# Optimization experiments

Hardware: AMD Instinct MI355X
Metric: run time of the kernel (lower is better)

The kernel has to match this reference:

```python
import jax, jax.numpy as jnp
import numpy as np

B = 128               # number of graphs in the batch
N_PER_GRAPH = 32768   # nodes per graph (equal-sized graphs -> static shapes)
N = B * N_PER_GRAPH
E = 4 * N
# PyG TopKPooling: k = ceil(ratio * nodes_in_graph)
K1, K2, K3 = 328, 33, 4  # ceil(0.01*32768), ceil(0.1*328), ceil(0.1*33)


def _topk_pool(x, w, k, num_graphs):
    """PyG TopKPooling (min_score=None, nonlinearity=tanh).
    score = tanh((x . w) / ||w||); keep top-k per graph; x_out = x[perm] * score[perm].
    Nodes are grouped contiguously per graph (sorted `batch`), equal graph sizes.
    """
    n = x.shape[0] // num_graphs
    s = jnp.tanh((x @ w) / jnp.linalg.norm(w))            # [N_cur]
    vals, idx = jax.lax.top_k(s.reshape(num_graphs, n), k)  # [B,k]
    xb = x.reshape(num_graphs, n, x.shape[-1])
    xs = jnp.take_along_axis(xb, idx[:, :, None], axis=1)   # gather kept nodes [B,k,F]
    return (xs * vals[:, :, None]).reshape(num_graphs * k, x.shape[-1])


def setup_inputs() -> dict:
    key = jax.random.key(0)
    ks = jax.random.split(key, 13)
    l1, l2, l3, l4 = 5, 64, 32, 8
    sc = 0.1
    return {
        "x": jax.random.normal(ks[0], (N, l1), jnp.float32),
        "edge_index": jax.random.randint(ks[1], (2, E), 0, N, jnp.int32),
        "batch": jnp.repeat(jnp.arange(B, dtype=jnp.int32), N_PER_GRAPH),
        "w1": jax.random.normal(ks[2], (l1,), jnp.float32) * sc,
        "W_ih": jax.random.normal(ks[3], (l2, l1), jnp.float32) * sc,
        "b_ih": jax.random.normal(ks[4], (l2,), jnp.float32) * sc,
        "b_hh": jax.random.normal(ks[5], (l2,), jnp.float32) * sc,
        "w2": jax.random.normal(ks[6], (l2,), jnp.float32) * sc,
        "W2": jax.random.normal(ks[7], (l3, l2), jnp.float32) * sc,
        "b2": jax.random.normal(ks[8], (l3,), jnp.float32) * sc,
        "w3": jax.random.normal(ks[9], (l3,), jnp.float32) * sc,
        "W3": jax.random.normal(ks[10], (l4, l3), jnp.float32) * sc,
        "b3": jax.random.normal(ks[11], (l4,), jnp.float32) * sc,
    }


def reference(x, edge_index, batch, w1, W_ih, b_ih, b_hh, w2, W2, b2, w3, W3, b3):
    # pool1 (ratio=0.01) -> RNNCell with h0=0: tanh(x W_ih^T + b_ih + b_hh)
    x = _topk_pool(x, w1, K1, B)
    x = jnp.tanh(x @ W_ih.T + b_ih + b_hh)
    # pool2 (ratio=0.1) -> relu(Linear)
    x = _topk_pool(x, w2, K2, B)
    x = jax.nn.relu(x @ W2.T + b2)
    # pool3 (ratio=0.1) -> Linear
    x = _topk_pool(x, w3, K3, B)
    return x @ W3.T + b3  # [B*K3, 8]
```

## Files before the change

kernel.cpp:

```cpp
#include <hip/hip_runtime.h>
#include <stdint.h>
#include <math.h>

constexpr int NPG = 32768;
constexpr int NGRAPH = 128;
constexpr int L1 = 5, L2 = 64, L3 = 32, L4 = 8;
constexpr int K1 = 328, K2 = 33, K3 = 4;
constexpr int SEGS = 16;
constexpr int CAP  = 64;

__device__ __forceinline__ uint32_t mono(float f) {
  uint32_t u = __float_as_uint(f);
  return (u & 0x80000000u) ? ~u : (u | 0x80000000u);
}
__device__ __forceinline__ float imono(uint32_t k) {
  uint32_t u = (k & 0x80000000u) ? (k ^ 0x80000000u) : ~k;
  return __uint_as_float(u);
}
__device__ __forceinline__ float fast_tanh(float x) {
  float e = __expf(2.0f * x);
  return 1.0f - 2.0f / (e + 1.0f);
}

__global__ __launch_bounds__(256) void score_kernel(
    const float* __restrict__ x, const float* __restrict__ w1,
    int* __restrict__ cnts, unsigned long long* __restrict__ cand) {
  __shared__ __align__(16) float sb[2048 * L1];
  __shared__ unsigned long long cb[CAP];
  __shared__ int s_n;
  __shared__ float s_tf;
  const int tid = threadIdx.x;
  const int g = blockIdx.x >> 4;
  const int bg = blockIdx.x & 15;
  if (tid == 0) {
    s_n = 0;
    float s = 0.f;
    for (int k = 0; k < L1; ++k) s += w1[k] * w1[k];
    s_tf = 2.2315f * sqrtf(s);
  }
  const float w10 = w1[0], w11 = w1[1], w12 = w1[2], w13 = w1[3], w14 = w1[4];
  const float4* src = (const float4*)(x + ((size_t)g * NPG + bg * 2048) * L1);
#pragma unroll
  for (int k = 0; k < 10; ++k)
    ((float4*)sb)[tid + 256 * k] = src[tid + 256 * k];
  __syncthreads();
  const float tf = s_tf;
#pragma unroll
  for (int p = 0; p < 4; ++p) {
    const int np = tid + 256 * p;
    const float* r = sb + np * 10;
    float d0 = r[0]*w10 + r[1]*w11 + r[2]*w12 + r[3]*w13 + r[4]*w14;
    float d1 = r[5]*w10 + r[6]*w11 + r[7]*w12 + r[8]*w13 + r[9]*w14;
    const int i0 = bg * 2048 + 2 * np;
    if (d0 >= tf) {
      int pos = atomicAdd(&s_n, 1);
      if (pos < CAP)
        cb[pos] = ((unsigned long long)mono(d0) << 16) | (unsigned)(65535 - i0);
    }
    if (d1 >= tf) {
      int pos = atomicAdd(&s_n, 1);
      if (pos < CAP)
        cb[pos] = ((unsigned long long)mono(d1) << 16) | (unsigned)(65535 - (i0 + 1));
    }
  }
  __syncthreads();
  const int n = s_n;
  if (tid == 0) cnts[g * SEGS + bg] = n;
  if (tid < CAP && tid < n)
    cand[((size_t)g * SEGS + bg) * CAP + tid] = cb[tid];
}

__global__ __launch_bounds__(1024, 1) void selmlp_kernel(
    const float* __restrict__ x, const int* __restrict__ cnts,
    const unsigned long long* __restrict__ cand,
    const float* __restrict__ w1, const float* __restrict__ W_ih,
    const float* __restrict__ b_ih, const float* __restrict__ b_hh,
    const float* __restrict__ w2, const float* __restrict__ W2,
    const float* __restrict__ b2, const float* __restrict__ w3,
    const float* __restrict__ W3, const float* __restrict__ b3,
    float* __restrict__ out) {
  __shared__ __align__(16) float hbuf[K1 * 65 + K2 * 68 + K2 * 33];
  __shared__ __align__(16) unsigned long long comp[1024];
  __shared__ __align__(16) unsigned long long sorted[512];
  __shared__ __align__(16) float fa[5672];
  __shared__ int soff[SEGS + 1];
  __shared__ int wred[16];
  __shared__ int s_fb, s_ctot, s_lo, s_hi, s_done, s_cnt;
  __shared__ uint32_t s_T;
  __shared__ float s_inv[3];

  float* xsel  = fa;
  float* sWihP = fa + 2624;
  float* sbih  = fa + 3136;
  float* sW2   = fa + 3200;
  float* sb2   = fa + 5280;
  float* sw2v  = fa + 5312;
  float* sw3v  = fa + 5376;
  float* sW3   = fa + 5408;
  float* sb3   = fa + 5664;

  const int tid = threadIdx.x;
  const int wid = tid >> 6;
  const int g = blockIdx.x;
  const float* xg = x + (size_t)g * NPG * L1;

  for (int i = tid; i < 512; i += 1024) {
    int o = i >> 3, k = i & 7;
    sWihP[i] = (k < L1) ? W_ih[o * L1 + k] : 0.f;
  }
  for (int i = tid; i < L2; i += 1024) { sbih[i] = b_ih[i] + b_hh[i]; sw2v[i] = w2[i]; }
  for (int i = tid; i < L3 * L2; i += 1024) sW2[(i >> 6) * 65 + (i & 63)] = W2[i];
  for (int i = tid; i < L3; i += 1024) { sb2[i] = b2[i]; sw3v[i] = w3[i]; }
  for (int i = tid; i < L4 * L3; i += 1024) sW3[i] = W3[i];
  for (int i = tid; i < L4; i += 1024) sb3[i] = b3[i];
  if (tid < 64) {
    float a = (tid < L1) ? w1[tid] : 0.f;
    float b = w2[tid];
    float c = (tid < L3) ? w3[tid] : 0.f;
    a *= a; b *= b; c *= c;
    for (int d = 1; d < 64; d <<= 1) {
      a += __shfl_xor(a, d); b += __shfl_xor(b, d); c += __shfl_xor(c, d);
    }
    if (tid == 0) {
      s_inv[0] = 1.f / sqrtf(a); s_inv[1] = 1.f / sqrtf(b); s_inv[2] = 1.f / sqrtf(c);
      s_cnt = 0; s_done = 0; s_lo = 0; s_hi = 0;
    }
  }
  if (tid < SEGS) soff[tid] = cnts[g * SEGS + tid];
  __syncthreads();
  if (tid == 0) {
    int off = 0, fb = 0;
    for (int s2 = 0; s2 < SEGS; ++s2) {
      int c = soff[s2];
      if (c > CAP) fb = 1;
      soff[s2] = off;
      off += c;
    }
    soff[SEGS] = off;
    if (off < K1 || off > 1024) fb = 1;
    s_fb = fb; s_ctot = off;
  }
  __syncthreads();

  if (!s_fb) {
    const int wl = tid & 63;
    if (wid < SEGS) {
      const int o = soff[wid], c = soff[wid + 1] - o;
      if (wl < c) comp[o + wl] = cand[((size_t)g * SEGS + wid) * CAP + wl];
    }
    const int ctot = s_ctot;
    const int nrk = (ctot + 7) & ~7;
    if (tid >= ctot && tid < nrk) comp[tid] = 0ULL;
    __syncthreads();
    if (tid < nrk) {
      unsigned long long c = comp[tid];
      int r = 0;
      for (int i = 0; i < nrk; i += 8) {
        ulonglong2 v0 = *(const ulonglong2*)&comp[i];
        ulonglong2 v1 = *(const ulonglong2*)&comp[i + 2];
        ulonglong2 v2 = *(const ulonglong2*)&comp[i + 4];
        ulonglong2 v3 = *(const ulonglong2*)&comp[i + 6];
        r += (v0.x > c) + (v0.y > c) + (v1.x > c) + (v1.y > c) +
             (v2.x > c) + (v2.y > c) + (v3.x > c) + (v3.y > c);
      }
      if (r < K1) sorted[r] = c;
    }
    __syncthreads();
  } else {
    const float w10 = w1[0], w11 = w1[1], w12 = w1[2], w13 = w1[3], w14 = w1[4];
    if (tid == 0) { s_lo = 0; s_hi = -1; s_done = 0; }
    __syncthreads();
    for (int it = 0; it < 36; ++it) {
      if (s_done) break;
      const uint32_t lo = (uint32_t)s_lo, hi = (uint32_t)s_hi;
      const uint32_t q = (uint32_t)(((unsigned long long)lo + (unsigned long long)hi) >> 1);
      int cc = 0;
      for (int m = 0; m < 32; ++m) {
        const int i = m * 1024 + tid;
        const float* r = xg + (size_t)i * L1;
        float dv = r[0]*w10 + r[1]*w11 + r[2]*w12 + r[3]*w13 + r[4]*w14;
        cc += (mono(dv) >= q);
      }
      for (int d = 1; d < 64; d <<= 1) cc += __shfl_xor(cc, d);
      if ((tid & 63) == 0) wred[wid] = cc;
      __syncthreads();
      if (tid == 0) {
        int tot = 0;
        for (int w = 0; w < 16; ++w) tot += wred[w];
        if (tot >= K1 && tot <= 1024) { s_T = q; s_done = 1; }
        else if ((uint32_t)s_hi - (uint32_t)s_lo <= 1u) { s_T = (uint32_t)s_lo; s_done = 1; }
        else if (tot > 1024) { s_lo = (int)q; }
        else                 { s_hi = (int)q; }
      }
      __syncthreads();
    }
    const uint32_t T = s_T;
    for (int m = 0; m < 32; ++m) {
      const int i = m * 1024 + tid;
      const float* r = xg + (size_t)i * L1;
      float dv = r[0]*w10 + r[1]*w11 + r[2]*w12 + r[3]*w13 + r[4]*w14;
      if (mono(dv) >= T) {
        int p = atomicAdd(&s_cnt, 1);
        if (p < 1024)
          comp[p] = ((unsigned long long)mono(dv) << 16) | (unsigned)(65535 - i);
      }
    }
    __syncthreads();
    int cnt = s_cnt; if (cnt > 1024) cnt = 1024;
    int nrk = (cnt + 7) & ~7; if (nrk < 8) nrk = 8;
    if (tid >= cnt && tid < nrk) comp[tid] = 0ULL;
    __syncthreads();
    if (tid < nrk) {
      unsigned long long c = comp[tid];
      int r = 0;
      for (int i = 0; i < nrk; i += 8) {
        ulonglong2 v0 = *(const ulonglong2*)&comp[i];
        ulonglong2 v1 = *(const ulonglong2*)&comp[i + 2];
        ulonglong2 v2 = *(const ulonglong2*)&comp[i + 4];
        ulonglong2 v3 = *(const ulonglong2*)&comp[i + 6];
        r += (v0.x > c) + (v0.y > c) + (v1.x > c) + (v1.y > c) +
             (v2.x > c) + (v2.y > c) + (v3.x > c) + (v3.y > c);
      }
      if (r < K1) sorted[r] = c;
    }
    __syncthreads();
  }

  const float inv1 = s_inv[0], inv2 = s_inv[1], inv3 = s_inv[2];

  for (int p = tid; p < K1 * 8; p += 1024) {
    int j = p >> 3, k = p & 7;
    unsigned long long c = sorted[j];
    int idx = 65535 - (int)(c & 0xFFFFu);
    float sc = fast_tanh(imono((uint32_t)(c >> 16)) * inv1);
    xsel[p] = (k < L1) ? xg[(size_t)idx * L1 + k] * sc : 0.f;
  }
  __syncthreads();
  {
    const int o = tid & 63;
    float wreg[8];
#pragma unroll
    for (int k = 0; k < 8; ++k) wreg[k] = sWihP[o * 8 + k];
    const float bias = sbih[o];
    for (int p = tid; p < K1 * L2; p += 1024) {
      int row = p >> 6;
      float4 xa = *(const float4*)&xsel[row * 8];
      float4 xb = *(const float4*)&xsel[row * 8 + 4];
      float acc = bias;
      acc += xa.x * wreg[0]; acc += xa.y * wreg[1]; acc += xa.z * wreg[2];
      acc += xa.w * wreg[3]; acc += xb.x * wreg[4]; acc += xb.y * wreg[5];
      acc += xb.z * wreg[6]; acc += xb.w * wreg[7];
      hbuf[row * 65 + o] = fast_tanh(acc);
    }
  }
  __syncthreads();

  for (int j = tid; j < 384; j += 1024) {
    unsigned long long c = 0ULL;
    if (j < K1) {
      const float* hr = hbuf + j * 65;
      float acc = 0.f;
      for (int k = 0; k < L2; ++k) acc += hr[k] * sw2v[k];
      c = ((unsigned long long)mono(acc) << 16) | (unsigned)(65535 - j);
    }
    comp[j] = c;
  }
  __syncthreads();
  if (tid < 384) {
    unsigned long long c = comp[tid];
    int r = 0;
    for (int i = 0; i < 384; i += 8) {
      ulonglong2 v0 = *(const ulonglong2*)&comp[i];
      ulonglong2 v1 = *(const ulonglong2*)&comp[i + 2];
      ulonglong2 v2 = *(const ulonglong2*)&comp[i + 4];
      ulonglong2 v3 = *(const ulonglong2*)&comp[i + 6];
      r += (v0.x > c) + (v0.y > c) + (v1.x > c) + (v1.y > c) +
           (v2.x > c) + (v2.y > c) + (v3.x > c) + (v3.y > c);
    }
    sorted[r] = c;
  }
  __syncthreads();

  float* x2f = hbuf + K1 * 65;
  for (int p = tid; p < K2 * L2; p += 1024) {
    int j = p >> 6, k = p & 63;
    unsigned long long c = sorted[j];
    int row = 65535 - (int)(c & 0xFFFFu);
    float sc = fast_tanh(imono((uint32_t)(c >> 16)) * inv2);
    x2f[j * 68 + k] = hbuf[row * 65 + k] * sc;
  }
  __syncthreads();

  float* yf = x2f + K2 * 68;
  for (int p = tid; p < K2 * L3; p += 1024) {
    int j = p >> 5, o = p & 31;
    const float4* xr4 = (const float4*)(x2f + j * 68);
    const float* wr = sW2 + o * 65;
    float acc = sb2[o];
#pragma unroll
    for (int m = 0; m < 16; ++m) {
      float4 v = xr4[m];
      acc += v.x * wr[4 * m];     acc += v.y * wr[4 * m + 1];
      acc += v.z * wr[4 * m + 2]; acc += v.w * wr[4 * m + 3];
    }
    yf[j * 33 + o] = fmaxf(acc, 0.f);
  }
  __syncthreads();

  for (int j = tid; j < 64; j += 1024) {
    unsigned long long c = 0ULL;
    if (j < K2) {
      const float* yr = yf + j * 33;
      float acc = 0.f;
      for (int k = 0; k < L3; ++k) acc += yr[k] * sw3v[k];
      c = ((unsigned long long)mono(acc) << 16) | (unsigned)(65535 - j);
    }
    comp[j] = c;
  }
  __syncthreads();
  if (tid < 64) {
    unsigned long long c = comp[tid];
    int r = 0;
    for (int i = 0; i < 64; i += 8) {
      ulonglong2 v0 = *(const ulonglong2*)&comp[i];
      ulonglong2 v1 = *(const ulonglong2*)&comp[i + 2];
      ulonglong2 v2 = *(const ulonglong2*)&comp[i + 4];
      ulonglong2 v3 = *(const ulonglong2*)&comp[i + 6];
      r += (v0.x > c) + (v0.y > c) + (v1.x > c) + (v1.y > c) +
           (v2.x > c) + (v2.y > c) + (v3.x > c) + (v3.y > c);
    }
    sorted[r] = c;
  }
  __syncthreads();

  for (int p = tid; p < K3 * L4; p += 1024) {
    int t = p >> 3, o = p & 7;
    unsigned long long c = sorted[t];
    int row = 65535 - (int)(c & 0xFFFFu);
    float sc = fast_tanh(imono((uint32_t)(c >> 16)) * inv3);
    const float* yr = yf + row * 33;
    const float* wr = sW3 + o * L3;
    float acc = sb3[o];
    for (int k = 0; k < L3; ++k) acc += yr[k] * sc * wr[k];
    out[((size_t)g * K3 + t) * L4 + o] = acc;
  }
}

extern "C" void kernel_launch(void* const* d_in, const int* in_sizes, int n_in,
                              void* d_out, int out_size, void* d_ws, size_t ws_size,
                              hipStream_t stream) {
  const float* x    = (const float*)d_in[0];
  const float* w1   = (const float*)d_in[3];
  const float* W_ih = (const float*)d_in[4];
  const float* b_ih = (const float*)d_in[5];
  const float* b_hh = (const float*)d_in[6];
  const float* w2   = (const float*)d_in[7];
  const float* W2   = (const float*)d_in[8];
  const float* b2   = (const float*)d_in[9];
  const float* w3   = (const float*)d_in[10];
  const float* W3   = (const float*)d_in[11];
  const float* b3   = (const float*)d_in[12];
  float* out = (float*)d_out;

  int* cnts = (int*)d_ws;
  unsigned long long* cand =
      (unsigned long long*)((char*)d_ws + 8192);

  score_kernel<<<dim3(NGRAPH * SEGS), dim3(256), 0, stream>>>(x, w1, cnts, cand);
  selmlp_kernel<<<dim3(NGRAPH), dim3(1024), 0, stream>>>(
      x, cnts, cand, w1, W_ih, b_ih, b_hh, w2, W2, b2, w3, W3, b3, out);
}
```

Measured before the change: 45.26 us.

## Fuse score and select/MLP stages into one cooperative kernel with grid sync

Replaces the two-kernel pipeline with one cooperative launch of 256 blocks of 1024 threads. Each pair of blocks scores half a graph, then a grid-wide sync hands off to one block per graph for selection and the MLP stages. The goal is to remove the second launch and the gap between kernels. The cost is fewer, larger blocks streaming x through LDS staging, plus a grid barrier, and it falls back to the old path if the cooperative launch fails.

After: 171.4 us. 3.79x slower.

```diff
diff --git a/kernel.cpp b/kernel.cpp
--- a/kernel.cpp
+++ b/kernel.cpp
@@ -1,13 +1,15 @@
 #include <hip/hip_runtime.h>
+#include <hip/hip_cooperative_groups.h>
 #include <stdint.h>
 #include <math.h>
+
+namespace cg = cooperative_groups;
 
 constexpr int NPG = 32768;
 constexpr int NGRAPH = 128;
 constexpr int L1 = 5, L2 = 64, L3 = 32, L4 = 8;
 constexpr int K1 = 328, K2 = 33, K3 = 4;
-constexpr int SEGS = 16;
-constexpr int CAP  = 64;
+constexpr int HCAP = 512;
 
 __device__ __forceinline__ uint32_t mono(float f) {
   uint32_t u = __float_as_uint(f);
@@ -21,6 +23,311 @@
   float e = __expf(2.0f * x);
   return 1.0f - 2.0f / (e + 1.0f);
 }
+
+__global__ __launch_bounds__(1024, 1) void fused_coop(
+    const float* __restrict__ x,
+    const float* __restrict__ w1, const float* __restrict__ W_ih,
+    const float* __restrict__ b_ih, const float* __restrict__ b_hh,
+    const float* __restrict__ w2, const float* __restrict__ W2,
+    const float* __restrict__ b2, const float* __restrict__ w3,
+    const float* __restrict__ W3, const float* __restrict__ b3,
+    int* __restrict__ cnts, unsigned long long* __restrict__ cand,
+    float* __restrict__ out) {
+  __shared__ __align__(16) float arena[33400];
+  __shared__ int wred[16];
+  __shared__ int s_n, s_fb, s_ctot, s_lo, s_hi, s_done, s_cnt, s_c0;
+  __shared__ uint32_t s_T;
+  __shared__ float s_inv[3], s_tf;
+
+  float* hbuf = arena;
+  unsigned long long* comp = (unsigned long long*)(arena + 24656);
+  unsigned long long* sorted = (unsigned long long*)(arena + 26704);
+  float* fa = arena + 27728;
+  float* xsel  = fa;
+  float* sWihP = fa + 2624;
+  float* sbih  = fa + 3136;
+  float* sW2   = fa + 3200;
+  float* sb2   = fa + 5280;
+  float* sw2v  = fa + 5312;
+  float* sw3v  = fa + 5376;
+  float* sW3   = fa + 5408;
+  float* sb3   = fa + 5664;
+
+  const int tid = threadIdx.x;
+  const int bid = blockIdx.x;
+  const int g1 = bid >> 1, half = bid & 1;
+
+  for (int i = tid; i < 512; i += 1024) {
+    int o = i >> 3, k = i & 7;
+    sWihP[i] = (k < L1) ? W_ih[o * L1 + k] : 0.f;
+  }
+  for (int i = tid; i < L2; i += 1024) { sbih[i] = b_ih[i] + b_hh[i]; sw2v[i] = w2[i]; }
+  for (int i = tid; i < L3 * L2; i += 1024) sW2[(i >> 6) * 65 + (i & 63)] = W2[i];
+  for (int i = tid; i < L3; i += 1024) { sb2[i] = b2[i]; sw3v[i] = w3[i]; }
+  for (int i = tid; i < L4 * L3; i += 1024) sW3[i] = W3[i];
+  for (int i = tid; i < L4; i += 1024) sb3[i] = b3[i];
+  if (tid < 64) {
+    float a = (tid < L1) ? w1[tid] : 0.f;
+    float b = w2[tid];
+    float c = (tid < L3) ? w3[tid] : 0.f;
+    a *= a; b *= b; c *= c;
+    for (int d = 1; d < 64; d <<= 1) {
+      a += __shfl_xor(a, d); b += __shfl_xor(b, d); c += __shfl_xor(c, d);
+    }
+    if (tid == 0) {
+      float nw1 = sqrtf(a);
+      s_tf = 2.2315f * nw1;
+      s_inv[0] = 1.f / nw1; s_inv[1] = 1.f / sqrtf(b); s_inv[2] = 1.f / sqrtf(c);
+      s_n = 0; s_cnt = 0; s_done = 0;
+    }
+  }
+  const float w10 = w1[0], w11 = w1[1], w12 = w1[2], w13 = w1[3], w14 = w1[4];
+
+  {
+    float* stage = arena;
+    unsigned long long* cb = (unsigned long long*)(arena + 20480);
+    const float4* src = (const float4*)(x + ((size_t)g1 * NPG + half * 16384) * L1);
+    __syncthreads();
+    const float tf = s_tf;
+    for (int c = 0; c < 4; ++c) {
+#pragma unroll
+      for (int q = 0; q < 5; ++q)
+        ((float4*)stage)[tid + 1024 * q] = src[c * 5120 + tid + 1024 * q];
+      __syncthreads();
+      const float* r = stage + tid * 20;
+      const int i0 = half * 16384 + c * 4096 + tid * 4;
+#pragma unroll
+      for (int n = 0; n < 4; ++n) {
+        float d = r[n*5]*w10 + r[n*5+1]*w11 + r[n*5+2]*w12 + r[n*5+3]*w13 + r[n*5+4]*w14;
+        if (d >= tf) {
+          int pos = atomicAdd(&s_n, 1);
+          if (pos < HCAP)
+            cb[pos] = ((unsigned long long)mono(d) << 16) | (unsigned)(65535 - (i0 + n));
+        }
+      }
+      __syncthreads();
+    }
+    const int n = s_n;
+    if (tid == 0) cnts[bid] = n;
+    if (tid < HCAP && tid < n) cand[(size_t)bid * HCAP + tid] = cb[tid];
+  }
+  __threadfence();
+  cg::this_grid().sync();
+  if (bid >= NGRAPH) return;
+
+  const int g = bid;
+  const float* xg = x + (size_t)g * NPG * L1;
+  __threadfence();
+  if (tid == 0) {
+    int c0 = cnts[2 * g], c1 = cnts[2 * g + 1];
+    int fb = (c0 > HCAP || c1 > HCAP) ? 1 : 0;
+    int tot = c0 + c1;
+    if (tot < K1 || tot > 1024) fb = 1;
+    s_fb = fb; s_ctot = tot; s_c0 = c0;
+    s_lo = 0; s_hi = -1; s_done = 0; s_cnt = 0;
+  }
+  __syncthreads();
+
+  if (!s_fb) {
+    const int ctot = s_ctot, c0 = s_c0;
+    if (tid < c0)            comp[tid] = cand[(size_t)(2 * g) * HCAP + tid];
+    else if (tid < ctot)     comp[tid] = cand[(size_t)(2 * g + 1) * HCAP + (tid - c0)];
+    const int nrk = (ctot + 7) & ~7;
+    if (tid >= ctot && tid < nrk) comp[tid] = 0ULL;
+    __syncthreads();
+    if (tid < nrk) {
+      unsigned long long c = comp[tid];
+      int r = 0;
+      for (int i = 0; i < nrk; i += 8) {
+        ulonglong2 v0 = *(const ulonglong2*)&comp[i];
+        ulonglong2 v1 = *(const ulonglong2*)&comp[i + 2];
+        ulonglong2 v2 = *(const ulonglong2*)&comp[i + 4];
+        ulonglong2 v3 = *(const ulonglong2*)&comp[i + 6];
+        r += (v0.x > c) + (v0.y > c) + (v1.x > c) + (v1.y > c) +
+             (v2.x > c) + (v2.y > c) + (v3.x > c) + (v3.y > c);
+      }
+      if (r < K1) sorted[r] = c;
+    }
+    __syncthreads();
+  } else {
+    for (int it = 0; it < 36; ++it) {
+      if (s_done) break;
+      const uint32_t lo = (uint32_t)s_lo, hi = (uint32_t)s_hi;
+      const uint32_t q = (uint32_t)(((unsigned long long)lo + (unsigned long long)hi) >> 1);
+      int cc = 0;
+      for (int m = 0; m < 32; ++m) {
+        const int i = m * 1024 + tid;
+        const float* r = xg + (size_t)i * L1;
+        float dv = r[0]*w10 + r[1]*w11 + r[2]*w12 + r[3]*w13 + r[4]*w14;
+        cc += (mono(dv) >= q);
+      }
+      for (int d = 1; d < 64; d <<= 1) cc += __shfl_xor(cc, d);
+      if ((tid & 63) == 0) wred[tid >> 6] = cc;
+      __syncthreads();
+      if (tid == 0) {
+        int tot = 0;
+        for (int w = 0; w < 16; ++w) tot += wred[w];
+        if (tot >= K1 && tot <= 1024) { s_T = q; s_done = 1; }
+        else if ((uint32_t)s_hi - (uint32_t)s_lo <= 1u) { s_T = (uint32_t)s_lo; s_done = 1; }
+        else if (tot > 1024) { s_lo = (int)q; }
+        else                 { s_hi = (int)q; }
+      }
+      __syncthreads();
+    }
+    const uint32_t T = s_T;
+    for (int m = 0; m < 32; ++m) {
+      const int i = m * 1024 + tid;
+      const float* r = xg + (size_t)i * L1;
+      float dv = r[0]*w10 + r[1]*w11 + r[2]*w12 + r[3]*w13 + r[4]*w14;
+      if (mono(dv) >= T) {
+        int p = atomicAdd(&s_cnt, 1);
+        if (p < 1024)
+          comp[p] = ((unsigned long long)mono(dv) << 16) | (unsigned)(65535 - i);
+      }
+    }
+    __syncthreads();
+    int cnt = s_cnt; if (cnt > 1024) cnt = 1024;
+    int nrk = (cnt + 7) & ~7; if (nrk < 8) nrk = 8;
+    if (tid >= cnt && tid < nrk) comp[tid] = 0ULL;
+    __syncthreads();
+    if (tid < nrk) {
+      unsigned long long c = comp[tid];
+      int r = 0;
+      for (int i = 0; i < nrk; i += 8) {
+        ulonglong2 v0 = *(const ulonglong2*)&comp[i];
+        ulonglong2 v1 = *(const ulonglong2*)&comp[i + 2];
+        ulonglong2 v2 = *(const ulonglong2*)&comp[i + 4];
+        ulonglong2 v3 = *(const ulonglong2*)&comp[i + 6];
+        r += (v0.x > c) + (v0.y > c) + (v1.x > c) + (v1.y > c) +
+             (v2.x > c) + (v2.y > c) + (v3.x > c) + (v3.y > c);
+      }
+      if (r < K1) sorted[r] = c;
+    }
+    __syncthreads();
+  }
+
+  const float inv1 = s_inv[0], inv2 = s_inv[1], inv3 = s_inv[2];
+
+  for (int p = tid; p < K1 * 8; p += 1024) {
+    int j = p >> 3, k = p & 7;
+    unsigned long long c = sorted[j];
+    int idx = 65535 - (int)(c & 0xFFFFu);
+    float sc = fast_tanh(imono((uint32_t)(c >> 16)) * inv1);
+    xsel[p] = (k < L1) ? xg[(size_t)idx * L1 + k] * sc : 0.f;
+  }
+  __syncthreads();
+  {
+    const int o = tid & 63;
+    float wreg[8];
+#pragma unroll
+    for (int k = 0; k < 8; ++k) wreg[k] = sWihP[o * 8 + k];
+    const float bias = sbih[o];
+    for (int p = tid; p < K1 * L2; p += 1024) {
+      int row = p >> 6;
+      float4 xa = *(const float4*)&xsel[row * 8];
+      float4 xb = *(const float4*)&xsel[row * 8 + 4];
+      float acc = bias;
+      acc += xa.x * wreg[0]; acc += xa.y * wreg[1]; acc += xa.z * wreg[2];
+      acc += xa.w * wreg[3]; acc += xb.x * wreg[4]; acc += xb.y * wreg[5];
+      acc += xb.z * wreg[6]; acc += xb.w * wreg[7];
+      hbuf[row * 65 + o] = fast_tanh(acc);
+    }
+  }
+  __syncthreads();
+
+  for (int j = tid; j < 384; j += 1024) {
+    unsigned long long c = 0ULL;
+    if (j < K1) {
+      const float* hr = hbuf + j * 65;
+      float acc = 0.f;
+      for (int k = 0; k < L2; ++k) acc += hr[k] * sw2v[k];
+      c = ((unsigned long long)mono(acc) << 16) | (unsigned)(65535 - j);
+    }
+    comp[j] = c;
+  }
+  __syncthreads();
+  if (tid < 384) {
+    unsigned long long c = comp[tid];
+    int r = 0;
+    for (int i = 0; i < 384; i += 8) {
+      ulonglong2 v0 = *(const ulonglong2*)&comp[i];
+      ulonglong2 v1 = *(const ulonglong2*)&comp[i + 2];
+      ulonglong2 v2 = *(const ulonglong2*)&comp[i + 4];
+      ulonglong2 v3 = *(const ulonglong2*)&comp[i + 6];
+      r += (v0.x > c) + (v0.y > c) + (v1.x > c) + (v1.y > c) +
+           (v2.x > c) + (v2.y > c) + (v3.x > c) + (v3.y > c);
+    }
+    sorted[r] = c;
+  }
+  __syncthreads();
+
+  float* x2f = hbuf + K1 * 65;
+  for (int p = tid; p < K2 * L2; p += 1024) {
+    int j = p >> 6, k = p & 63;
+    unsigned long long c = sorted[j];
+    int row = 65535 - (int)(c & 0xFFFFu);
+    float sc = fast_tanh(imono((uint32_t)(c >> 16)) * inv2);
+    x2f[j * 68 + k] = hbuf[row * 65 + k] * sc;
+  }
+  __syncthreads();
+
+  float* yf = x2f + K2 * 68;
+  for (int p = tid; p < K2 * L3; p += 1024) {
+    int j = p >> 5, o = p & 31;
+    const float4* xr4 = (const float4*)(x2f + j * 68);
+    const float* wr = sW2 + o * 65;
+    float acc = sb2[o];
+#pragma unroll
+    for (int m = 0; m < 16; ++m) {
+      float4 v = xr4[m];
+      acc += v.x * wr[4 * m];     acc += v.y * wr[4 * m + 1];
+      acc += v.z * wr[4 * m + 2]; acc += v.w * wr[4 * m + 3];
+    }
+    yf[j * 33 + o] = fmaxf(acc, 0.f);
+  }
+  __syncthreads();
+
+  for (int j = tid; j < 64; j += 1024) {
+    unsigned long long c = 0ULL;
+    if (j < K2) {
+      const float* yr = yf + j * 33;
+      float acc = 0.f;
+      for (int k = 0; k < L3; ++k) acc += yr[k] * sw3v[k];
+      c = ((unsigned long long)mono(acc) << 16) | (unsigned)(65535 - j);
+    }
+    comp[j] = c;
+  }
+  __syncthreads();
+  if (tid < 64) {
+    unsigned long long c = comp[tid];
+    int r = 0;
+    for (int i = 0; i < 64; i += 8) {
+      ulonglong2 v0 = *(const ulonglong2*)&comp[i];
+      ulonglong2 v1 = *(const ulonglong2*)&comp[i + 2];
+      ulonglong2 v2 = *(const ulonglong2*)&comp[i + 4];
+      ulonglong2 v3 = *(const ulonglong2*)&comp[i + 6];
+      r += (v0.x > c) + (v0.y > c) + (v1.x > c) + (v1.y > c) +
+           (v2.x > c) + (v2.y > c) + (v3.x > c) + (v3.y > c);
+    }
+    sorted[r] = c;
+  }
+  __syncthreads();
+
+  for (int p = tid; p < K3 * L4; p += 1024) {
+    int t = p >> 3, o = p & 7;
+    unsigned long long c = sorted[t];
+    int row = 65535 - (int)(c & 0xFFFFu);
+    float sc = fast_tanh(imono((uint32_t)(c >> 16)) * inv3);
+    const float* yr = yf + row * 33;
+    const float* wr = sW3 + o * L3;
+    float acc = sb3[o];
+    for (int k = 0; k < L3; ++k) acc += yr[k] * sc * wr[k];
+    out[((size_t)g * K3 + t) * L4 + o] = acc;
+  }
+}
+
+constexpr int SEGS = 16;
+constexpr int CAP  = 64;
 
 __global__ __launch_bounds__(256) void score_kernel(
     const float* __restrict__ x, const float* __restrict__ w1,
@@ -366,7 +673,15 @@
   unsigned long long* cand =
       (unsigned long long*)((char*)d_ws + 8192);
 
-  score_kernel<<<dim3(NGRAPH * SEGS), dim3(256), 0, stream>>>(x, w1, cnts, cand);
-  selmlp_kernel<<<dim3(NGRAPH), dim3(1024), 0, stream>>>(
-      x, cnts, cand, w1, W_ih, b_ih, b_hh, w2, W2, b2, w3, W3, b3, out);
+  void* args[] = { (void*)&x, (void*)&w1, (void*)&W_ih, (void*)&b_ih,
+                   (void*)&b_hh, (void*)&w2, (void*)&W2, (void*)&b2,
+                   (void*)&w3, (void*)&W3, (void*)&b3,
+                   (void*)&cnts, (void*)&cand, (void*)&out };
+  hipError_t err = hipLaunchCooperativeKernel(
+      (const void*)fused_coop, dim3(2 * NGRAPH), dim3(1024), args, 0, stream);
+  if (err != hipSuccess) {
+    score_kernel<<<dim3(NGRAPH * SEGS), dim3(256), 0, stream>>>(x, w1, cnts, cand);
+    selmlp_kernel<<<dim3(NGRAPH), dim3(1024), 0, stream>>>(
+        x, cnts, cand, w1, W_ih, b_ih, b_hh, w2, W2, b2, w3, W3, b3, out);
+  }
 }
```

## Compute RNN hidden states and pool2 scores for candidates in score kernel

Applied to the files above, without the earlier changes.

The score kernel now evaluates the RNNCell (tanh of W_ih·x plus bias) and the pool2 score for every top-k candidate it finds, spread across all 2048 blocks. It writes the hidden states and scores to a workspace slot per candidate. The per-graph selection kernel then runs pool2 directly on those precomputed scores and gathers only the 33 kept hidden rows, skipping its serial xsel/hidden-layer phases. The cost is extra global traffic: writing hidden vectors for all candidates, not just the 328 kept ones. The path also depends on the workspace being large enough, and falls back to the old path otherwise.

New measurement: 49.99 us. 1.1x slower.

```diff
diff --git a/kernel.cpp b/kernel.cpp
--- a/kernel.cpp
+++ b/kernel.cpp
@@ -8,6 +8,7 @@
 constexpr int K1 = 328, K2 = 33, K3 = 4;
 constexpr int SEGS = 16;
 constexpr int CAP  = 64;
+constexpr int SLOTS = SEGS * CAP;
 
 __device__ __forceinline__ uint32_t mono(float f) {
   uint32_t u = __float_as_uint(f);
@@ -24,11 +25,18 @@
 
 __global__ __launch_bounds__(256) void score_kernel(
     const float* __restrict__ x, const float* __restrict__ w1,
-    int* __restrict__ cnts, unsigned long long* __restrict__ cand) {
+    const float* __restrict__ W_ih, const float* __restrict__ b_ih,
+    const float* __restrict__ b_hh, const float* __restrict__ w2,
+    int* __restrict__ cnts, unsigned long long* __restrict__ cand,
+    float* __restrict__ s2g, float* __restrict__ hG, int hasH) {
   __shared__ __align__(16) float sb[2048 * L1];
   __shared__ unsigned long long cb[CAP];
+  __shared__ float xs[CAP * L1];
+  __shared__ float sWih[L2 * L1];
+  __shared__ float sbih[L2];
+  __shared__ float sw2[L2];
   __shared__ int s_n;
-  __shared__ float s_tf;
+  __shared__ float s_tf, s_inv1;
   const int tid = threadIdx.x;
   const int g = blockIdx.x >> 4;
   const int bg = blockIdx.x & 15;
@@ -36,8 +44,12 @@
     s_n = 0;
     float s = 0.f;
     for (int k = 0; k < L1; ++k) s += w1[k] * w1[k];
-    s_tf = 2.2315f * sqrtf(s);
-  }
+    float nw = sqrtf(s);
+    s_tf = 2.2315f * nw;
+    s_inv1 = 1.f / nw;
+  }
+  for (int i = tid; i < L2 * L1; i += 256) sWih[i] = W_ih[i];
+  for (int i = tid; i < L2; i += 256) { sbih[i] = b_ih[i] + b_hh[i]; sw2[i] = w2[i]; }
   const float w10 = w1[0], w11 = w1[1], w12 = w1[2], w13 = w1[3], w14 = w1[4];
   const float4* src = (const float4*)(x + ((size_t)g * NPG + bg * 2048) * L1);
 #pragma unroll
@@ -65,14 +77,40 @@
   }
   __syncthreads();
   const int n = s_n;
+  const int nn = n < CAP ? n : CAP;
   if (tid == 0) cnts[g * SEGS + bg] = n;
   if (tid < CAP && tid < n)
     cand[((size_t)g * SEGS + bg) * CAP + tid] = cb[tid];
+  if (!hasH) return;
+  for (int p = tid; p < nn * L1; p += 256) {
+    int ci = p / L1, k = p - ci * L1;
+    unsigned long long c = cb[ci];
+    int i = 65535 - (int)(c & 0xFFFFu);
+    int local = i - bg * 2048;
+    float sc = fast_tanh(imono((uint32_t)(c >> 16)) * s_inv1);
+    xs[p] = sb[local * L1 + k] * sc;
+  }
+  __syncthreads();
+  for (int p = tid; p < nn * 64; p += 256) {
+    int ci = p >> 6, o = p & 63;
+    const float* xr = xs + ci * L1;
+    const float* wr = sWih + o * L1;
+    float acc = sbih[o];
+#pragma unroll
+    for (int k = 0; k < L1; ++k) acc += xr[k] * wr[k];
+    float h = fast_tanh(acc);
+    const int slot = bg * CAP + ci;
+    hG[((size_t)g * SLOTS + slot) * 64 + o] = h;
+    float term = h * sw2[o];
+    for (int d = 1; d < 64; d <<= 1) term += __shfl_xor(term, d);
+    if (o == 0) s2g[(size_t)g * SLOTS + slot] = term;
+  }
 }
 
 __global__ __launch_bounds__(1024, 1) void selmlp_kernel(
     const float* __restrict__ x, const int* __restrict__ cnts,
     const unsigned long long* __restrict__ cand,
+    const float* __restrict__ s2g, const float* __restrict__ hG, int hasH,
     const float* __restrict__ w1, const float* __restrict__ W_ih,
     const float* __restrict__ b_ih, const float* __restrict__ b_hh,
     const float* __restrict__ w2, const float* __restrict__ W2,
@@ -83,6 +121,8 @@
   __shared__ __align__(16) unsigned long long comp[1024];
   __shared__ __align__(16) unsigned long long sorted[512];
   __shared__ __align__(16) float fa[5672];
+  __shared__ int slotarr[1024];
+  __shared__ int slotof[512];
   __shared__ int soff[SEGS + 1];
   __shared__ int wred[16];
   __shared__ int s_fb, s_ctot, s_lo, s_hi, s_done, s_cnt;
@@ -129,7 +169,7 @@
   if (tid < SEGS) soff[tid] = cnts[g * SEGS + tid];
   __syncthreads();
   if (tid == 0) {
-    int off = 0, fb = 0;
+    int off = 0, fb = hasH ? 0 : 1;
     for (int s2 = 0; s2 < SEGS; ++s2) {
       int c = soff[s2];
       if (c > CAP) fb = 1;
@@ -142,11 +182,18 @@
   }
   __syncthreads();
 
+  const float inv1 = s_inv[0], inv2 = s_inv[1], inv3 = s_inv[2];
+  float* x2f = hbuf + K1 * 65;
+  float* yf  = x2f + K2 * 68;
+
   if (!s_fb) {
     const int wl = tid & 63;
     if (wid < SEGS) {
       const int o = soff[wid], c = soff[wid + 1] - o;
-      if (wl < c) comp[o + wl] = cand[((size_t)g * SEGS + wid) * CAP + wl];
+      if (wl < c) {
+        comp[o + wl] = cand[((size_t)g * SEGS + wid) * CAP + wl];
+        slotarr[o + wl] = wid * CAP + wl;
+      }
     }
     const int ctot = s_ctot;
     const int nrk = (ctot + 7) & ~7;
@@ -163,7 +210,38 @@
         r += (v0.x > c) + (v0.y > c) + (v1.x > c) + (v1.y > c) +
              (v2.x > c) + (v2.y > c) + (v3.x > c) + (v3.y > c);
       }
-      if (r < K1) sorted[r] = c;
+      if (r < K1) slotof[r] = slotarr[tid];
+    }
+    __syncthreads();
+    for (int j = tid; j < 384; j += 1024) {
+      unsigned long long c = 0ULL;
+      if (j < K1) {
+        float s2 = s2g[(size_t)g * SLOTS + slotof[j]];
+        c = ((unsigned long long)mono(s2) << 16) | (unsigned)(65535 - j);
+      }
+      comp[j] = c;
+    }
+    __syncthreads();
+    if (tid < 384) {
+      unsigned long long c = comp[tid];
+      int r = 0;
+      for (int i = 0; i < 384; i += 8) {
+        ulonglong2 v0 = *(const ulonglong2*)&comp[i];
+        ulonglong2 v1 = *(const ulonglong2*)&comp[i + 2];
+        ulonglong2 v2 = *(const ulonglong2*)&comp[i + 4];
+        ulonglong2 v3 = *(const ulonglong2*)&comp[i + 6];
+        r += (v0.x > c) + (v0.y > c) + (v1.x > c) + (v1.y > c) +
+             (v2.x > c) + (v2.y > c) + (v3.x > c) + (v3.y > c);
+      }
+      sorted[r] = c;
+    }
+    __syncthreads();
+    for (int p = tid; p < K2 * L2; p += 1024) {
+      int j = p >> 6, k = p & 63;
+      unsigned long long c = sorted[j];
+      int row = 65535 - (int)(c & 0xFFFFu);
+      float sc = fast_tanh(imono((uint32_t)(c >> 16)) * inv2);
+      x2f[j * 68 + k] = hG[((size_t)g * SLOTS + slotof[row]) * 64 + k] * sc;
     }
     __syncthreads();
   } else {
@@ -224,74 +302,67 @@
       if (r < K1) sorted[r] = c;
     }
     __syncthreads();
-  }
-
-  const float inv1 = s_inv[0], inv2 = s_inv[1], inv3 = s_inv[2];
-
-  for (int p = tid; p < K1 * 8; p += 1024) {
-    int j = p >> 3, k = p & 7;
-    unsigned long long c = sorted[j];
-    int idx = 65535 - (int)(c & 0xFFFFu);
-    float sc = fast_tanh(imono((uint32_t)(c >> 16)) * inv1);
-    xsel[p] = (k < L1) ? xg[(size_t)idx * L1 + k] * sc : 0.f;
-  }
-  __syncthreads();
-  {
-    const int o = tid & 63;
-    float wreg[8];
+    for (int p = tid; p < K1 * 8; p += 1024) {
+      int j = p >> 3, k = p & 7;
+      unsigned long long c = sorted[j];
+      int idx = 65535 - (int)(c & 0xFFFFu);
+      float sc = fast_tanh(imono((uint32_t)(c >> 16)) * inv1);
+      xsel[p] = (k < L1) ? xg[(size_t)idx * L1 + k] * sc : 0.f;
+    }
+    __syncthreads();
+    {
+      const int o = tid & 63;
+      float wreg[8];
 #pragma unroll
-    for (int k = 0; k < 8; ++k) wreg[k] = sWihP[o * 8 + k];
-    const float bias = sbih[o];
-    for (int p = tid; p < K1 * L2; p += 1024) {
-      int row = p >> 6;
-      float4 xa = *(const float4*)&xsel[row * 8];
-      float4 xb = *(const float4*)&xsel[row * 8 + 4];
-      float acc = bias;
-      acc += xa.x * wreg[0]; acc += xa.y * wreg[1]; acc += xa.z * wreg[2];
-      acc += xa.w * wreg[3]; acc += xb.x * wreg[4]; acc += xb.y * wreg[5];
-      acc += xb.z * wreg[6]; acc += xb.w * wreg[7];
-      hbuf[row * 65 + o] = fast_tanh(acc);
-    }
-  }
-  __syncthreads();
-
-  for (int j = tid; j < 384; j += 1024) {
-    unsigned long long c = 0ULL;
-    if (j < K1) {
-      const float* hr = hbuf + j * 65;
-      float acc = 0.f;
-      for (int k = 0; k < L2; ++k) acc += hr[k] * sw2v[k];
-      c = ((unsigned long long)mono(acc) << 16) | (unsigned)(65535 - j);
-    }
-    comp[j] = c;
-  }
-  __syncthreads();
-  if (tid < 384) {
-    unsigned long long c = comp[tid];
-    int r = 0;
-    for (int i = 0; i < 384; i += 8) {
-      ulonglong2 v0 = *(const ulonglong2*)&comp[i];
-      ulonglong2 v1 = *(const ulonglong2*)&comp[i + 2];
-      ulonglong2 v2 = *(const ulonglong2*)&comp[i + 4];
-      ulonglong2 v3 = *(const ulonglong2*)&comp[i + 6];
-      r += (v0.x > c) + (v0.y > c) + (v1.x > c) + (v1.y > c) +
-           (v2.x > c) + (v2.y > c) + (v3.x > c) + (v3.y > c);
-    }
-    sorted[r] = c;
-  }
-  __syncthreads();
-
-  float* x2f = hbuf + K1 * 65;
-  for (int p = tid; p < K2 * L2; p += 1024) {
-    int j = p >> 6, k = p & 63;
-    unsigned long long c = sorted[j];
-    int row = 65535 - (int)(c & 0xFFFFu);
-    float sc = fast_tanh(imono((uint32_t)(c >> 16)) * inv2);
-    x2f[j * 68 + k] = hbuf[row * 65 + k] * sc;
-  }
-  __syncthreads();
-
-  float* yf = x2f + K2 * 68;
+      for (int k = 0; k < 8; ++k) wreg[k] = sWihP[o * 8 + k];
+      const float bias = sbih[o];
+      for (int p = tid; p < K1 * L2; p += 1024) {
+        int row = p >> 6;
+        float4 xa = *(const float4*)&xsel[row * 8];
+        float4 xb = *(const float4*)&xsel[row * 8 + 4];
+        float acc = bias;
+        acc += xa.x * wreg[0]; acc += xa.y * wreg[1]; acc += xa.z * wreg[2];
+        acc += xa.w * wreg[3]; acc += xb.x * wreg[4]; acc += xb.y * wreg[5];
+        acc += xb.z * wreg[6]; acc += xb.w * wreg[7];
+        hbuf[row * 65 + o] = fast_tanh(acc);
+      }
+    }
+    __syncthreads();
+    for (int j = tid; j < 384; j += 1024) {
+      unsigned long long c = 0ULL;
+      if (j < K1) {
+        const float* hr = hbuf + j * 65;
+        float acc = 0.f;
+        for (int k = 0; k < L2; ++k) acc += hr[k] * sw2v[k];
+        c = ((unsigned long long)mono(acc) << 16) | (unsigned)(65535 - j);
+      }
+      comp[j] = c;
+    }
+    __syncthreads();
+    if (tid < 384) {
+      unsigned long long c = comp[tid];
+      int r = 0;
+      for (int i = 0; i < 384; i += 8) {
+        ulonglong2 v0 = *(const ulonglong2*)&comp[i];
+        ulonglong2 v1 = *(const ulonglong2*)&comp[i + 2];
+        ulonglong2 v2 = *(const ulonglong2*)&comp[i + 4];
+        ulonglong2 v3 = *(const ulonglong2*)&comp[i + 6];
+        r += (v0.x > c) + (v0.y > c) + (v1.x > c) + (v1.y > c) +
+             (v2.x > c) + (v2.y > c) + (v3.x > c) + (v3.y > c);
+      }
+      sorted[r] = c;
+    }
+    __syncthreads();
+    for (int p = tid; p < K2 * L2; p += 1024) {
+      int j = p >> 6, k = p & 63;
+      unsigned long long c = sorted[j];
+      int row = 65535 - (int)(c & 0xFFFFu);
+      float sc = fast_tanh(imono((uint32_t)(c >> 16)) * inv2);
+      x2f[j * 68 + k] = hbuf[row * 65 + k] * sc;
+    }
+    __syncthreads();
+  }
+
   for (int p = tid; p < K2 * L3; p += 1024) {
     int j = p >> 5, o = p & 31;
     const float4* xr4 = (const float4*)(x2f + j * 68);
@@ -362,11 +433,19 @@
   const float* b3   = (const float*)d_in[12];
   float* out = (float*)d_out;
 
+  const size_t cnts_b = (size_t)NGRAPH * SEGS * sizeof(int);
+  const size_t cand_b = (size_t)NGRAPH * SLOTS * sizeof(unsigned long long);
+  const size_t s2_b   = (size_t)NGRAPH * SLOTS * sizeof(float);
+  const size_t h_b    = (size_t)NGRAPH * SLOTS * 64 * sizeof(float);
   int* cnts = (int*)d_ws;
-  unsigned long long* cand =
-      (unsigned long long*)((char*)d_ws + 8192);
-
-  score_kernel<<<dim3(NGRAPH * SEGS), dim3(256), 0, stream>>>(x, w1, cnts, cand);
+  unsigned long long* cand = (unsigned long long*)((char*)d_ws + cnts_b);
+  float* s2g = (float*)((char*)d_ws + cnts_b + cand_b);
+  float* hG  = (float*)((char*)d_ws + cnts_b + cand_b + s2_b);
+  const int hasH = (ws_size >= cnts_b + cand_b + s2_b + h_b) ? 1 : 0;
+
+  score_kernel<<<dim3(NGRAPH * SEGS), dim3(256), 0, stream>>>(
+      x, w1, W_ih, b_ih, b_hh, w2, cnts, cand, s2g, hG, hasH);
   selmlp_kernel<<<dim3(NGRAPH), dim3(1024), 0, stream>>>(
-      x, cnts, cand, w1, W_ih, b_ih, b_hh, w2, W2, b2, w3, W3, b3, out);
-}
+      x, cnts, cand, s2g, hG, hasH,
+      w1, W_ih, b_ih, b_hh, w2, W2, b2, w3, W3, b3, out);
+}
```
